# Kernel optimization log

Hardware: AMD Instinct MI355X
Metric: run time of the kernel (lower is better)

## Reference

```python
import jax, jax.numpy as jnp
import numpy as np

N_NODES = 50000
N_EDGES = 400000
B = 2
NUM_STEP = 2
# SAGEConv layer dims (in, out): conv1..conv6
LAYER_DIMS = [(64, 128), (128, 64), (64, 32), (32, 32), (64, 64), (128, 64)]


def setup_inputs() -> dict:
    key = jax.random.key(0)
    ks = jax.random.split(key, 4 + 3 * len(LAYER_DIMS))
    inp = {
        "in_feat": jax.random.normal(ks[0], (B, N_NODES, 64), dtype=jnp.float32),
        "src": jax.random.randint(ks[1], (N_EDGES,), 0, N_NODES, dtype=jnp.int32),
        "dst": jax.random.randint(ks[2], (N_EDGES,), 0, N_NODES, dtype=jnp.int32),
    }
    for i, (fin, fout) in enumerate(LAYER_DIMS, start=1):
        scale = jnp.float32(1.0 / np.sqrt(fin))
        inp[f"w_self{i}"] = jax.random.normal(ks[3 * i], (fin, fout), dtype=jnp.float32) * scale
        inp[f"w_neigh{i}"] = jax.random.normal(ks[3 * i + 1], (fin, fout), dtype=jnp.float32) * scale
        inp[f"b{i}"] = jnp.zeros((fout,), dtype=jnp.float32)
    return inp


def reference(in_feat, src, dst,
              w_self1, w_neigh1, b1, w_self2, w_neigh2, b2,
              w_self3, w_neigh3, b3, w_self4, w_neigh4, b4,
              w_self5, w_neigh5, b5, w_self6, w_neigh6, b6):
    # in_feat: [B, N, F] -> internal [N, B, F] (matches torch transpose(0,1))
    h = jnp.transpose(in_feat, (1, 0, 2))
    # in-degree per dst node for mean aggregation (0-degree nodes -> agg 0)
    deg = jax.ops.segment_sum(jnp.ones(src.shape[0], jnp.float32), dst,
                              num_segments=N_NODES)
    deg = jnp.maximum(deg, 1.0)[:, None, None]  # [N,1,1]

    def sage(x, ws, wn, b):
        # DGL SAGEConv (mean): fc_self(h) + fc_neigh(mean_{u in N(v)} h_u) + b
        agg = jax.ops.segment_sum(x[src], dst, num_segments=N_NODES) / deg
        return x @ ws + agg @ wn + b

    for _ in range(NUM_STEP):
        h1 = jax.nn.relu(sage(h, w_self1, w_neigh1, b1))
        h2 = jax.nn.relu(sage(h1, w_self2, w_neigh2, b2))
        h3 = jax.nn.relu(sage(h2, w_self3, w_neigh3, b3))
        h4 = jnp.concatenate(
            [jax.nn.relu(sage(h3, w_self4, w_neigh4, b4)), h3], axis=2)
        h5 = jnp.concatenate(
            [jax.nn.relu(sage(h4, w_self5, w_neigh5, b5)), h4], axis=2)
        h = sage(h5, w_self6, w_neigh6, b6)
    return jnp.transpose(h, (1, 0, 2))
```

## Files before the change

kernel.cpp:

```cpp
#include <hip/hip_runtime.h>

#define NN 50000
#define NE 400000
#define BB 2
#define ROWS (NN * BB)

#define SCAN_CHUNK 1024
#define SCAN_NB ((NN + SCAN_CHUNK - 1) / SCAN_CHUNK)

__device__ inline void fma4(float4& a, float s, const float4& w) {
    a.x = fmaf(s, w.x, a.x); a.y = fmaf(s, w.y, a.y);
    a.z = fmaf(s, w.z, a.z); a.w = fmaf(s, w.w, a.w);
}
__device__ inline void add4(float4& a, const float4& v) {
    a.x += v.x; a.y += v.y; a.z += v.z; a.w += v.w;
}
__device__ inline unsigned bf2(float a, float b) {
    unsigned ua = __float_as_uint(a); ua = (ua + 0x7FFFu + ((ua >> 16) & 1u)) >> 16;
    unsigned ub = __float_as_uint(b); ub = (ub + 0x7FFFu + ((ub >> 16) & 1u)) >> 16;
    return ua | (ub << 16);
}
__device__ inline void bfadd(float4& lo, float4& hi, uint4 v) {
    lo.x += __uint_as_float(v.x << 16); lo.y += __uint_as_float(v.x & 0xFFFF0000u);
    lo.z += __uint_as_float(v.y << 16); lo.w += __uint_as_float(v.y & 0xFFFF0000u);
    hi.x += __uint_as_float(v.z << 16); hi.y += __uint_as_float(v.z & 0xFFFF0000u);
    hi.z += __uint_as_float(v.w << 16); hi.w += __uint_as_float(v.w & 0xFFFF0000u);
}


__global__ void k_hist(const int* __restrict__ dst, int* __restrict__ deg) {
    int e = blockIdx.x * 256 + threadIdx.x;
    if (e < NE) atomicAdd(&deg[dst[e]], 1);
}

__global__ __launch_bounds__(256) void k_scan1(const int* __restrict__ deg,
                                               int* __restrict__ bsum) {
    int b = blockIdx.x, t = threadIdx.x;
    int base = b * SCAN_CHUNK + t * 4;
    int s = 0;
#pragma unroll
    for (int i = 0; i < 4; i++) {
        int idx = base + i;
        if (idx < NN) s += deg[idx];
    }
    for (int d = 32; d; d >>= 1) s += __shfl_down(s, d);
    __shared__ int ws[4];
    if ((t & 63) == 0) ws[t >> 6] = s;
    __syncthreads();
    if (t == 0) bsum[b] = ws[0] + ws[1] + ws[2] + ws[3];
}

__global__ void k_scan2(const int* __restrict__ bsum, int* __restrict__ boff,
                        int* __restrict__ rowoff_last) {
    int lane = threadIdx.x;
    int v = (lane < SCAN_NB) ? bsum[lane] : 0;
    int incl = v;
    for (int d = 1; d < 64; d <<= 1) {
        int o = __shfl_up(incl, d);
        if (lane >= d) incl += o;
    }
    if (lane < SCAN_NB) boff[lane] = incl - v;
    if (lane == 63) rowoff_last[0] = incl;
}

__global__ __launch_bounds__(256) void k_scan3(const int* __restrict__ deg,
                                               const int* __restrict__ boff,
                                               int* __restrict__ rowoff,
                                               int* __restrict__ cursor,
                                               float* __restrict__ rdeg) {
    int b = blockIdx.x, t = threadIdx.x;
    int lane = t & 63, wv = t >> 6;
    int base = b * SCAN_CHUNK + t * 4;
    int dv[4];
    int ts = 0;
#pragma unroll
    for (int i = 0; i < 4; i++) {
        int idx = base + i;
        dv[i] = (idx < NN) ? deg[idx] : 0;
        ts += dv[i];
    }
    int incl = ts;
    for (int d = 1; d < 64; d <<= 1) {
        int o = __shfl_up(incl, d);
        if (lane >= d) incl += o;
    }
    __shared__ int wsum[4];
    if (lane == 63) wsum[wv] = incl;
    __syncthreads();
    int wexc = 0;
    for (int w = 0; w < wv; w++) wexc += wsum[w];
    int run = boff[b] + wexc + (incl - ts);
#pragma unroll
    for (int i = 0; i < 4; i++) {
        int idx = base + i;
        if (idx < NN) {
            rowoff[idx] = run;
            cursor[idx] = run;
            rdeg[idx] = 1.0f / fmaxf((float)dv[i], 1.0f);
            run += dv[i];
        }
    }
}

__global__ void k_fill(const int* __restrict__ src, const int* __restrict__ dst,
                       int* __restrict__ cursor, int* __restrict__ csr) {
    int e = blockIdx.x * 256 + threadIdx.x;
    if (e >= NE) return;
    int pos = atomicAdd(&cursor[dst[e]], 1);
    csr[pos] = src[e];
}


__global__ void k_gather(const float4* __restrict__ x, const int* __restrict__ csr,
                         const int* __restrict__ rowoff, const float* __restrict__ rdeg,
                         float4* __restrict__ out, int w4s,
                         int xns4, int xbs4, int xo4, int op4, int oo4) {
    int t = blockIdx.x * 256 + threadIdx.x;
    int n = t >> w4s, tid = t & ((1 << w4s) - 1);
    if (n >= NN) return;
    int beg = rowoff[n], end = rowoff[n + 1];
    int a0 = xo4 + tid;
    float4 c00 = {0.f,0.f,0.f,0.f}, c01 = {0.f,0.f,0.f,0.f};
    float4 c10 = {0.f,0.f,0.f,0.f}, c11 = {0.f,0.f,0.f,0.f};
    int j = beg;
    for (; j + 4 <= end; j += 4) {
        int s0 = csr[j], s1 = csr[j+1], s2 = csr[j+2], s3 = csr[j+3];
        int b0 = s0 * xns4 + a0, b1 = s1 * xns4 + a0;
        int b2 = s2 * xns4 + a0, b3 = s3 * xns4 + a0;
        float4 p0 = x[b0], q0 = x[b0 + xbs4];
        float4 p1 = x[b1], q1 = x[b1 + xbs4];
        float4 p2 = x[b2], q2 = x[b2 + xbs4];
        float4 p3 = x[b3], q3 = x[b3 + xbs4];
        add4(c00, p0); add4(c10, q0); add4(c01, p1); add4(c11, q1);
        add4(c00, p2); add4(c10, q2); add4(c01, p3); add4(c11, q3);
    }
    for (; j < end; j++) {
        int s = csr[j];
        int b = s * xns4 + a0;
        add4(c00, x[b]); add4(c10, x[b + xbs4]);
    }
    float rd = rdeg[n];
    float4 o0 = {(c00.x+c01.x)*rd, (c00.y+c01.y)*rd, (c00.z+c01.z)*rd, (c00.w+c01.w)*rd};
    float4 o1 = {(c10.x+c11.x)*rd, (c10.y+c11.y)*rd, (c10.z+c11.z)*rd, (c10.w+c11.w)*rd};
    out[(2*n)     * op4 + oo4 + tid] = o0;
    out[(2*n + 1) * op4 + oo4 + tid] = o1;
}

__global__ void k_gather_bf(const uint4* __restrict__ x, const int* __restrict__ csr,
                            const int* __restrict__ rowoff, const float* __restrict__ rdeg,
                            float4* __restrict__ out, int w8s, int op4, int oo4) {
    int t = blockIdx.x * 256 + threadIdx.x;
    int n = t >> w8s, tid = t & ((1 << w8s) - 1);
    if (n >= NN) return;
    int rp8 = 1 << w8s, nrp = 2 << w8s;
    int beg = rowoff[n], end = rowoff[n + 1];
    float4 a0l = {0.f,0.f,0.f,0.f}, a0h = {0.f,0.f,0.f,0.f};
    float4 a1l = {0.f,0.f,0.f,0.f}, a1h = {0.f,0.f,0.f,0.f};
    int j = beg;
    for (; j + 2 <= end; j += 2) {
        int s0 = csr[j], s1 = csr[j+1];
        int b0 = s0 * nrp + tid, b1 = s1 * nrp + tid;
        uint4 p0 = x[b0], q0 = x[b0 + rp8];
        uint4 p1 = x[b1], q1 = x[b1 + rp8];
        bfadd(a0l, a0h, p0); bfadd(a1l, a1h, q0);
        bfadd(a0l, a0h, p1); bfadd(a1l, a1h, q1);
    }
    if (j < end) {
        int s = csr[j];
        int b = s * nrp + tid;
        bfadd(a0l, a0h, x[b]); bfadd(a1l, a1h, x[b + rp8]);
    }
    float rd = rdeg[n];
    float4 o0l = {a0l.x*rd, a0l.y*rd, a0l.z*rd, a0l.w*rd};
    float4 o0h = {a0h.x*rd, a0h.y*rd, a0h.z*rd, a0h.w*rd};
    float4 o1l = {a1l.x*rd, a1l.y*rd, a1l.z*rd, a1l.w*rd};
    float4 o1h = {a1h.x*rd, a1h.y*rd, a1h.z*rd, a1h.w*rd};
    int r0 = (2*n) * op4 + oo4 + 2*tid;
    int r1 = (2*n + 1) * op4 + oo4 + 2*tid;
    out[r0] = o0l; out[r0 + 1] = o0h;
    out[r1] = o1l; out[r1 + 1] = o1h;
}

template<int FIN, int FOUT, int MODE, bool RELU, bool TRANS, int RPT, int NCQ, int CS, bool OBF>
__global__ __launch_bounds__(256) void k_gemm(
    const float* __restrict__ x, const float* __restrict__ agg,
    const float* __restrict__ w0, const float* __restrict__ w1,
    const float* __restrict__ bias, float* __restrict__ out,
    int xns4, int xbs4, int xo4, int apitch4, int aoff4, int ostride4, int ooff4)
{
    constexpr int NQ = FOUT / 4;
    constexpr int NQB = NQ / CS;
    constexpr int TX = NQB / NCQ;
    constexpr int TY = 256 / TX;
    constexpr int TM = TY * RPT;
    constexpr int W4B = FIN * NQB;
    constexpr int NW = (MODE == 1) ? 2 : 1;

    __shared__ float4 wlds[NW * W4B];

    int t = threadIdx.x;
    int cq0 = blockIdx.y * NQB;
    const float4* w0v = (const float4*)w0;
    for (int i = t; i < W4B; i += 256)
        wlds[i] = w0v[(i / NQB) * NQ + cq0 + (i % NQB)];
    if (MODE == 1) {
        const float4* w1v = (const float4*)w1;
        for (int i = t; i < W4B; i += 256)
            wlds[W4B + i] = w1v[(i / NQB) * NQ + cq0 + (i % NQB)];
    }
    __syncthreads();

    int tx = t % TX, ty = t / TX;
    int rbase = blockIdx.x * TM + ty * RPT;

    int xb[RPT], ab[RPT];
#pragma unroll
    for (int i = 0; i < RPT; i++) {
        int r = rbase + i;
        r = r < ROWS ? r : ROWS - 1;
        xb[i] = (r >> 1) * xns4 + (r & 1) * xbs4 + xo4;
        ab[i] = r * apitch4 + aoff4;
    }

    float4 acc[RPT][NCQ];
#pragma unroll
    for (int i = 0; i < RPT; i++)
#pragma unroll
        for (int j = 0; j < NCQ; j++) acc[i][j] = make_float4(0.f, 0.f, 0.f, 0.f);

    const float4* xv4 = (const float4*)x;
    const float4* av4 = (const float4*)agg;

    for (int k4 = 0; k4 < FIN / 4; k4++) {
        float4 wq[4][NCQ], nq[4][NCQ];
#pragma unroll
        for (int u = 0; u < 4; u++)
#pragma unroll
            for (int j = 0; j < NCQ; j++) {
                wq[u][j] = wlds[(k4 * 4 + u) * NQB + tx + j * TX];
                if (MODE == 1) nq[u][j] = wlds[W4B + (k4 * 4 + u) * NQB + tx + j * TX];
            }
#pragma unroll
        for (int i = 0; i < RPT; i++) {
            float4 xv = xv4[xb[i] + k4];
#pragma unroll
            for (int j = 0; j < NCQ; j++) {
                fma4(acc[i][j], xv.x, wq[0][j]); fma4(acc[i][j], xv.y, wq[1][j]);
                fma4(acc[i][j], xv.z, wq[2][j]); fma4(acc[i][j], xv.w, wq[3][j]);
            }
            if (MODE == 1) {
                float4 av = av4[ab[i] + k4];
#pragma unroll
                for (int j = 0; j < NCQ; j++) {
                    fma4(acc[i][j], av.x, nq[0][j]); fma4(acc[i][j], av.y, nq[1][j]);
                    fma4(acc[i][j], av.z, nq[2][j]); fma4(acc[i][j], av.w, nq[3][j]);
                }
            }
        }
    }

    float4 b4[NCQ];
#pragma unroll
    for (int j = 0; j < NCQ; j++) {
        b4[j] = make_float4(0.f, 0.f, 0.f, 0.f);
        if (MODE != 0) b4[j] = *(const float4*)&bias[(cq0 + tx + j * TX) * 4];
    }

#pragma unroll
    for (int i = 0; i < RPT; i++) {
        int r = rbase + i;
        if (r >= ROWS) continue;
#pragma unroll
        for (int j = 0; j < NCQ; j++) {
            int q = cq0 + tx + j * TX;
            float4 v = acc[i][j];
            if (MODE == 2) {
                float4 ag = av4[ab[i] + q];
                add4(v, ag);
            }
            if (MODE != 0) add4(v, b4[j]);
            if (RELU) {
                v.x = fmaxf(v.x, 0.f); v.y = fmaxf(v.y, 0.f);
                v.z = fmaxf(v.z, 0.f); v.w = fmaxf(v.w, 0.f);
            }
            if (OBF) {
                uint2 w; w.x = bf2(v.x, v.y); w.y = bf2(v.z, v.w);
                ((uint2*)out)[r * ostride4 + ooff4 + q] = w;
            } else {
                int oidx;
                if (TRANS) {
                    int n = r >> 1, b = r & 1;
                    oidx = b * (NN * 16) + n * 16 + q;
                } else {
                    oidx = r * ostride4 + ooff4 + q;
                }
                ((float4*)out)[oidx] = v;
            }
        }
    }
}


template<int FIN, int FOUT, int MODE, bool RELU, bool TRANS,
         int RPT = 8, int NCQ = 1, int CS = 1, bool OBF = false>
static void launch_gemm(const float* x, const float* agg, const float* w0, const float* w1,
                        const float* bias, float* out, int xns4, int xbs4, int xo4,
                        int apitch4, int aoff4, int ostride4, int ooff4,
                        hipStream_t stream) {
    constexpr int TM = (256 / (FOUT / 4 / CS / NCQ)) * RPT;
    int nb = (ROWS + TM - 1) / TM;
    k_gemm<FIN, FOUT, MODE, RELU, TRANS, RPT, NCQ, CS, OBF>
        <<<dim3(nb, CS), 256, 0, stream>>>(
        x, agg, w0, w1, bias, out, xns4, xbs4, xo4, apitch4, aoff4, ostride4, ooff4);
}

static void launch_gather(const float* x, const int* csr, const int* rowoff,
                          const float* rdeg, float* aggb, int width,
                          int xns4, int xbs4, int xo4, int op4, int oo4,
                          hipStream_t stream) {
    int w4s = 0;
    while ((1 << w4s) < width / 4) w4s++;
    int gt = NN << w4s;
    k_gather<<<(gt + 255) / 256, 256, 0, stream>>>(
        (const float4*)x, csr, rowoff, rdeg, (float4*)aggb, w4s,
        xns4, xbs4, xo4, op4, oo4);
}

static void launch_gather_bf(const float* z, const int* csr, const int* rowoff,
                             const float* rdeg, float* aggb, int width,
                             int op4, int oo4, hipStream_t stream) {
    int w8s = 0;
    while ((1 << w8s) < width / 8) w8s++;
    int gt = NN << w8s;
    k_gather_bf<<<(gt + 255) / 256, 256, 0, stream>>>(
        (const uint4*)z, csr, rowoff, rdeg, (float4*)aggb, w8s, op4, oo4);
}

extern "C" void kernel_launch(void* const* d_in, const int* in_sizes, int n_in,
                              void* d_out, int out_size, void* d_ws, size_t ws_size,
                              hipStream_t stream) {
    const float* in_feat = (const float*)d_in[0];
    const int* src = (const int*)d_in[1];
    const int* dst = (const int*)d_in[2];
    const float* Ws[6], *Wn[6], *Bi[6];
    for (int i = 0; i < 6; i++) {
        Ws[i] = (const float*)d_in[3 + 3 * i];
        Wn[i] = (const float*)d_in[4 + 3 * i];
        Bi[i] = (const float*)d_in[5 + 3 * i];
    }

    char* ws = (char*)d_ws;
    size_t off = 0;
    auto alloc = [&](size_t bytes) {
        void* p = ws + off;
        off = (off + bytes + 255) & ~(size_t)255;
        return p;
    };
    float* rdeg   = (float*)alloc((size_t)NN * 4);
    int*   deg    = (int*)  alloc((size_t)NN * 4);
    int*   rowoff = (int*)  alloc((size_t)(NN + 1) * 4);
    int*   cursor = (int*)  alloc((size_t)NN * 4);
    int*   csr    = (int*)  alloc((size_t)NE * 4);
    int*   bsum   = (int*)  alloc((size_t)SCAN_NB * 4);
    int*   boff   = (int*)  alloc((size_t)SCAN_NB * 4);
    float* bufH   = (float*)alloc((size_t)ROWS * 64 * 4);
    float* bufA   = (float*)alloc((size_t)ROWS * 128 * 4);
    float* bufB   = (float*)alloc((size_t)ROWS * 128 * 4);
    float* aggb   = (float*)alloc((size_t)ROWS * 64 * 4);
    float* zbuf   = (float*)d_out;

    hipMemsetAsync(deg, 0, (size_t)NN * 4, stream);
    k_hist<<<(NE + 255) / 256, 256, 0, stream>>>(dst, deg);
    k_scan1<<<SCAN_NB, 256, 0, stream>>>(deg, bsum);
    k_scan2<<<1, 64, 0, stream>>>(bsum, boff, rowoff + NN);
    k_scan3<<<SCAN_NB, 256, 0, stream>>>(deg, boff, rowoff, cursor, rdeg);
    k_fill<<<(NE + 255) / 256, 256, 0, stream>>>(src, dst, cursor, csr);

    const int BSTR = NN * 16;

    for (int s = 0; s < 2; s++) {
        int last = (s == 1);
        const float* hx = s ? bufH : in_feat;
        int hns = s ? 32 : 16, hbs = s ? 16 : BSTR;

        launch_gather(hx, csr, rowoff, rdeg, aggb, 64, hns, hbs, 0, 16, 0, stream);
        launch_gemm<64, 128, 1, true, false, 8, 2, 2>(hx, aggb, Ws[0], Wn[0], Bi[0],
                                                      bufA, hns, hbs, 0, 16, 0, 32, 0, stream);

        launch_gemm<128, 64, 0, false, false, 8, 2, 1, true>(
            bufA, nullptr, Wn[1], nullptr, nullptr, zbuf, 64, 32, 0, 0, 0, 16, 0, stream);
        launch_gather_bf(zbuf, csr, rowoff, rdeg, aggb, 64, 16, 0, stream);
        launch_gemm<128, 64, 2, true, false, 8, 2>(bufA, aggb, Ws[1], nullptr, Bi[1],
                                                   bufH, 64, 32, 0, 16, 0, 16, 0, stream);

        launch_gemm<64, 32, 0, false, false, 8, 1, 1, true>(
            bufH, nullptr, Wn[2], nullptr, nullptr, zbuf, 32, 16, 0, 0, 0, 8, 0, stream);
        launch_gather_bf(zbuf, csr, rowoff, rdeg, aggb, 32, 8, 0, stream);
        launch_gemm<64, 32, 2, true, false, 8, 1>(bufH, aggb, Ws[2], nullptr, Bi[2],
                                                  bufB, 32, 16, 0, 8, 0, 32, 24, stream);

        launch_gather(bufB, csr, rowoff, rdeg, aggb, 32, 64, 32, 24, 16, 8, stream);
        launch_gemm<32, 32, 1, true, false, 8, 1>(bufB, aggb, Ws[3], Wn[3], Bi[3],
                                                  bufB, 64, 32, 24, 16, 8, 32, 16, stream);

        launch_gather(bufB, csr, rowoff, rdeg, aggb, 32, 64, 32, 16, 16, 0, stream);
        launch_gemm<64, 64, 1, true, false, 8, 2>(bufB, aggb, Ws[4], Wn[4], Bi[4],
                                                  bufB, 64, 32, 16, 16, 0, 32, 0, stream);

        launch_gemm<128, 64, 0, false, false, 8, 2, 1, true>(
            bufB, nullptr, Wn[5], nullptr, nullptr, zbuf, 64, 32, 0, 0, 0, 16, 0, stream);
        launch_gather_bf(zbuf, csr, rowoff, rdeg, aggb, 64, 16, 0, stream);
        if (last) {
            launch_gemm<128, 64, 2, false, true, 8, 2>(bufB, aggb, Ws[5], nullptr, Bi[5],
                                                       (float*)d_out, 64, 32, 0, 16, 0, 16, 0, stream);
        } else {
            launch_gemm<128, 64, 2, false, false, 8, 2>(bufB, aggb, Ws[5], nullptr, Bi[5],
                                                        bufH, 64, 32, 0, 16, 0, 16, 0, stream);
        }
    }
}
```

Measured before the change: 1.108 ms.

## Gather all neighbor features from bf16 copies written by GEMM epilogues

Drops the fp32 gather kernel. Every neighbor aggregation now reads bf16 packed features: a pack kernel converts the input once, and the GEMM epilogues gain a DUAL mode that also writes a bf16 copy of their output. The aim is to roughly halve the bytes read in the random-access gathers for layers 1, 4 and 5 and for step 2's input. The column-split (CS) grid dimension in the GEMM is also removed. The cost is bf16 rounding in more aggregations plus extra epilogue stores, and bufA is reused as scratch for the bf16 copies.

```diff
diff --git a/kernel.cpp b/kernel.cpp
--- a/kernel.cpp
+++ b/kernel.cpp
@@ -111,64 +111,44 @@
 }
 
 
-__global__ void k_gather(const float4* __restrict__ x, const int* __restrict__ csr,
-                         const int* __restrict__ rowoff, const float* __restrict__ rdeg,
-                         float4* __restrict__ out, int w4s,
-                         int xns4, int xbs4, int xo4, int op4, int oo4) {
+__global__ void k_pack(const float4* __restrict__ in, uint4* __restrict__ out) {
     int t = blockIdx.x * 256 + threadIdx.x;
-    int n = t >> w4s, tid = t & ((1 << w4s) - 1);
-    if (n >= NN) return;
-    int beg = rowoff[n], end = rowoff[n + 1];
-    int a0 = xo4 + tid;
-    float4 c00 = {0.f,0.f,0.f,0.f}, c01 = {0.f,0.f,0.f,0.f};
-    float4 c10 = {0.f,0.f,0.f,0.f}, c11 = {0.f,0.f,0.f,0.f};
-    int j = beg;
-    for (; j + 4 <= end; j += 4) {
-        int s0 = csr[j], s1 = csr[j+1], s2 = csr[j+2], s3 = csr[j+3];
-        int b0 = s0 * xns4 + a0, b1 = s1 * xns4 + a0;
-        int b2 = s2 * xns4 + a0, b3 = s3 * xns4 + a0;
-        float4 p0 = x[b0], q0 = x[b0 + xbs4];
-        float4 p1 = x[b1], q1 = x[b1 + xbs4];
-        float4 p2 = x[b2], q2 = x[b2 + xbs4];
-        float4 p3 = x[b3], q3 = x[b3 + xbs4];
-        add4(c00, p0); add4(c10, q0); add4(c01, p1); add4(c11, q1);
-        add4(c00, p2); add4(c10, q2); add4(c01, p3); add4(c11, q3);
-    }
-    for (; j < end; j++) {
-        int s = csr[j];
-        int b = s * xns4 + a0;
-        add4(c00, x[b]); add4(c10, x[b + xbs4]);
-    }
-    float rd = rdeg[n];
-    float4 o0 = {(c00.x+c01.x)*rd, (c00.y+c01.y)*rd, (c00.z+c01.z)*rd, (c00.w+c01.w)*rd};
-    float4 o1 = {(c10.x+c11.x)*rd, (c10.y+c11.y)*rd, (c10.z+c11.z)*rd, (c10.w+c11.w)*rd};
-    out[(2*n)     * op4 + oo4 + tid] = o0;
-    out[(2*n + 1) * op4 + oo4 + tid] = o1;
+    if (t >= ROWS * 8) return;
+    int r = t >> 3, k = t & 7;
+    int n = r >> 1, b = r & 1;
+    float4 a = in[(b * NN + n) * 16 + k * 2];
+    float4 c = in[(b * NN + n) * 16 + k * 2 + 1];
+    uint4 o;
+    o.x = bf2(a.x, a.y); o.y = bf2(a.z, a.w);
+    o.z = bf2(c.x, c.y); o.w = bf2(c.z, c.w);
+    out[t] = o;
 }
 
 __global__ void k_gather_bf(const uint4* __restrict__ x, const int* __restrict__ csr,
                             const int* __restrict__ rowoff, const float* __restrict__ rdeg,
-                            float4* __restrict__ out, int w8s, int op4, int oo4) {
+                            float4* __restrict__ out, int w8s, int xp8, int xo8,
+                            int op4, int oo4) {
     int t = blockIdx.x * 256 + threadIdx.x;
     int n = t >> w8s, tid = t & ((1 << w8s) - 1);
     if (n >= NN) return;
-    int rp8 = 1 << w8s, nrp = 2 << w8s;
     int beg = rowoff[n], end = rowoff[n + 1];
+    int a0 = xo8 + tid;
+    int xp2 = 2 * xp8;
     float4 a0l = {0.f,0.f,0.f,0.f}, a0h = {0.f,0.f,0.f,0.f};
     float4 a1l = {0.f,0.f,0.f,0.f}, a1h = {0.f,0.f,0.f,0.f};
     int j = beg;
     for (; j + 2 <= end; j += 2) {
         int s0 = csr[j], s1 = csr[j+1];
-        int b0 = s0 * nrp + tid, b1 = s1 * nrp + tid;
-        uint4 p0 = x[b0], q0 = x[b0 + rp8];
-        uint4 p1 = x[b1], q1 = x[b1 + rp8];
+        int b0 = s0 * xp2 + a0, b1 = s1 * xp2 + a0;
+        uint4 p0 = x[b0], q0 = x[b0 + xp8];
+        uint4 p1 = x[b1], q1 = x[b1 + xp8];
         bfadd(a0l, a0h, p0); bfadd(a1l, a1h, q0);
         bfadd(a0l, a0h, p1); bfadd(a1l, a1h, q1);
     }
     if (j < end) {
         int s = csr[j];
-        int b = s * nrp + tid;
-        bfadd(a0l, a0h, x[b]); bfadd(a1l, a1h, x[b + rp8]);
+        int b = s * xp2 + a0;
+        bfadd(a0l, a0h, x[b]); bfadd(a1l, a1h, x[b + xp8]);
     }
     float rd = rdeg[n];
     float4 o0l = {a0l.x*rd, a0l.y*rd, a0l.z*rd, a0l.w*rd};
@@ -181,32 +161,29 @@
     out[r1] = o1l; out[r1 + 1] = o1h;
 }
 
-template<int FIN, int FOUT, int MODE, bool RELU, bool TRANS, int RPT, int NCQ, int CS, bool OBF>
+template<int FIN, int FOUT, int MODE, bool RELU, bool TRANS, int RPT, int NCQ, bool OBF, bool DUAL>
 __global__ __launch_bounds__(256) void k_gemm(
     const float* __restrict__ x, const float* __restrict__ agg,
     const float* __restrict__ w0, const float* __restrict__ w1,
     const float* __restrict__ bias, float* __restrict__ out,
-    int xns4, int xbs4, int xo4, int apitch4, int aoff4, int ostride4, int ooff4)
+    int xns4, int xbs4, int xo4, int apitch4, int aoff4, int ostride4, int ooff4,
+    uint2* __restrict__ bfo, int bfp2, int bfo2)
 {
     constexpr int NQ = FOUT / 4;
-    constexpr int NQB = NQ / CS;
-    constexpr int TX = NQB / NCQ;
+    constexpr int TX = NQ / NCQ;
     constexpr int TY = 256 / TX;
     constexpr int TM = TY * RPT;
-    constexpr int W4B = FIN * NQB;
+    constexpr int W4 = FIN * NQ;
     constexpr int NW = (MODE == 1) ? 2 : 1;
 
-    __shared__ float4 wlds[NW * W4B];
+    __shared__ float4 wlds[NW * W4];
 
     int t = threadIdx.x;
-    int cq0 = blockIdx.y * NQB;
     const float4* w0v = (const float4*)w0;
-    for (int i = t; i < W4B; i += 256)
-        wlds[i] = w0v[(i / NQB) * NQ + cq0 + (i % NQB)];
+    for (int i = t; i < W4; i += 256) wlds[i] = w0v[i];
     if (MODE == 1) {
         const float4* w1v = (const float4*)w1;
-        for (int i = t; i < W4B; i += 256)
-            wlds[W4B + i] = w1v[(i / NQB) * NQ + cq0 + (i % NQB)];
+        for (int i = t; i < W4; i += 256) wlds[W4 + i] = w1v[i];
     }
     __syncthreads();
 
@@ -237,8 +214,8 @@
         for (int u = 0; u < 4; u++)
 #pragma unroll
             for (int j = 0; j < NCQ; j++) {
-                wq[u][j] = wlds[(k4 * 4 + u) * NQB + tx + j * TX];
-                if (MODE == 1) nq[u][j] = wlds[W4B + (k4 * 4 + u) * NQB + tx + j * TX];
+                wq[u][j] = wlds[(k4 * 4 + u) * NQ + tx + j * TX];
+                if (MODE == 1) nq[u][j] = wlds[W4 + (k4 * 4 + u) * NQ + tx + j * TX];
             }
 #pragma unroll
         for (int i = 0; i < RPT; i++) {
@@ -263,7 +240,7 @@
 #pragma unroll
     for (int j = 0; j < NCQ; j++) {
         b4[j] = make_float4(0.f, 0.f, 0.f, 0.f);
-        if (MODE != 0) b4[j] = *(const float4*)&bias[(cq0 + tx + j * TX) * 4];
+        if (MODE != 0) b4[j] = *(const float4*)&bias[(tx + j * TX) * 4];
     }
 
 #pragma unroll
@@ -272,7 +249,7 @@
         if (r >= ROWS) continue;
 #pragma unroll
         for (int j = 0; j < NCQ; j++) {
-            int q = cq0 + tx + j * TX;
+            int q = tx + j * TX;
             float4 v = acc[i][j];
             if (MODE == 2) {
                 float4 ag = av4[ab[i] + q];
@@ -296,44 +273,37 @@
                 }
                 ((float4*)out)[oidx] = v;
             }
+            if (DUAL) {
+                uint2 w; w.x = bf2(v.x, v.y); w.y = bf2(v.z, v.w);
+                bfo[r * bfp2 + bfo2 + q] = w;
+            }
         }
     }
 }
 
 
 template<int FIN, int FOUT, int MODE, bool RELU, bool TRANS,
-         int RPT = 8, int NCQ = 1, int CS = 1, bool OBF = false>
+         int RPT = 8, int NCQ = 1, bool OBF = false, bool DUAL = false>
 static void launch_gemm(const float* x, const float* agg, const float* w0, const float* w1,
                         const float* bias, float* out, int xns4, int xbs4, int xo4,
                         int apitch4, int aoff4, int ostride4, int ooff4,
-                        hipStream_t stream) {
-    constexpr int TM = (256 / (FOUT / 4 / CS / NCQ)) * RPT;
+                        hipStream_t stream,
+                        uint2* bfo = nullptr, int bfp2 = 0, int bfo2 = 0) {
+    constexpr int TM = (256 / (FOUT / 4 / NCQ)) * RPT;
     int nb = (ROWS + TM - 1) / TM;
-    k_gemm<FIN, FOUT, MODE, RELU, TRANS, RPT, NCQ, CS, OBF>
-        <<<dim3(nb, CS), 256, 0, stream>>>(
-        x, agg, w0, w1, bias, out, xns4, xbs4, xo4, apitch4, aoff4, ostride4, ooff4);
-}
-
-static void launch_gather(const float* x, const int* csr, const int* rowoff,
-                          const float* rdeg, float* aggb, int width,
-                          int xns4, int xbs4, int xo4, int op4, int oo4,
-                          hipStream_t stream) {
-    int w4s = 0;
-    while ((1 << w4s) < width / 4) w4s++;
-    int gt = NN << w4s;
-    k_gather<<<(gt + 255) / 256, 256, 0, stream>>>(
-        (const float4*)x, csr, rowoff, rdeg, (float4*)aggb, w4s,
-        xns4, xbs4, xo4, op4, oo4);
-}
-
-static void launch_gather_bf(const float* z, const int* csr, const int* rowoff,
+    k_gemm<FIN, FOUT, MODE, RELU, TRANS, RPT, NCQ, OBF, DUAL><<<nb, 256, 0, stream>>>(
+        x, agg, w0, w1, bias, out, xns4, xbs4, xo4, apitch4, aoff4, ostride4, ooff4,
+        bfo, bfp2, bfo2);
+}
+
+static void launch_gather_bf(const void* xbf, const int* csr, const int* rowoff,
                              const float* rdeg, float* aggb, int width,
-                             int op4, int oo4, hipStream_t stream) {
+                             int xp8, int xo8, int op4, int oo4, hipStream_t stream) {
     int w8s = 0;
     while ((1 << w8s) < width / 8) w8s++;
     int gt = NN << w8s;
     k_gather_bf<<<(gt + 255) / 256, 256, 0, stream>>>(
-        (const uint4*)z, csr, rowoff, rdeg, (float4*)aggb, w8s, op4, oo4);
+        (const uint4*)xbf, csr, rowoff, rdeg, (float4*)aggb, w8s, xp8, xo8, op4, oo4);
 }
 
 extern "C" void kernel_launch(void* const* d_in, const int* in_sizes, int n_in,
@@ -369,6 +339,9 @@
     float* aggb   = (float*)alloc((size_t)ROWS * 64 * 4);
     float* zbuf   = (float*)d_out;
 
+    uint2* hbf  = (uint2*)bufA;
+    uint2* b3bf = (uint2*)(bufA + (size_t)ROWS * 32);
+
     hipMemsetAsync(deg, 0, (size_t)NN * 4, stream);
     k_hist<<<(NE + 255) / 256, 256, 0, stream>>>(dst, deg);
     k_scan1<<<SCAN_NB, 256, 0, stream>>>(deg, bsum);
@@ -376,6 +349,8 @@
     k_scan3<<<SCAN_NB, 256, 0, stream>>>(deg, boff, rowoff, cursor, rdeg);
     k_fill<<<(NE + 255) / 256, 256, 0, stream>>>(src, dst, cursor, csr);
 
+    k_pack<<<(ROWS * 8 + 255) / 256, 256, 0, stream>>>((const float4*)in_feat, (uint4*)hbf);
+
     const int BSTR = NN * 16;
 
     for (int s = 0; s < 2; s++) {
@@ -383,39 +358,42 @@
         const float* hx = s ? bufH : in_feat;
         int hns = s ? 32 : 16, hbs = s ? 16 : BSTR;
 
-        launch_gather(hx, csr, rowoff, rdeg, aggb, 64, hns, hbs, 0, 16, 0, stream);
-        launch_gemm<64, 128, 1, true, false, 8, 2, 2>(hx, aggb, Ws[0], Wn[0], Bi[0],
-                                                      bufA, hns, hbs, 0, 16, 0, 32, 0, stream);
-
-        launch_gemm<128, 64, 0, false, false, 8, 2, 1, true>(
+        launch_gather_bf(hbf, csr, rowoff, rdeg, aggb, 64, 8, 0, 16, 0, stream);
+        launch_gemm<64, 128, 1, true, false, 8, 2>(hx, aggb, Ws[0], Wn[0], Bi[0],
+                                                   bufA, hns, hbs, 0, 16, 0, 32, 0, stream);
+
+        launch_gemm<128, 64, 0, false, false, 8, 2, true>(
             bufA, nullptr, Wn[1], nullptr, nullptr, zbuf, 64, 32, 0, 0, 0, 16, 0, stream);
-        launch_gather_bf(zbuf, csr, rowoff, rdeg, aggb, 64, 16, 0, stream);
+        launch_gather_bf(zbuf, csr, rowoff, rdeg, aggb, 64, 8, 0, 16, 0, stream);
         launch_gemm<128, 64, 2, true, false, 8, 2>(bufA, aggb, Ws[1], nullptr, Bi[1],
                                                    bufH, 64, 32, 0, 16, 0, 16, 0, stream);
 
-        launch_gemm<64, 32, 0, false, false, 8, 1, 1, true>(
+        launch_gemm<64, 32, 0, false, false, 8, 1, true>(
             bufH, nullptr, Wn[2], nullptr, nullptr, zbuf, 32, 16, 0, 0, 0, 8, 0, stream);
-        launch_gather_bf(zbuf, csr, rowoff, rdeg, aggb, 32, 8, 0, stream);
-        launch_gemm<64, 32, 2, true, false, 8, 1>(bufH, aggb, Ws[2], nullptr, Bi[2],
-                                                  bufB, 32, 16, 0, 8, 0, 32, 24, stream);
-
-        launch_gather(bufB, csr, rowoff, rdeg, aggb, 32, 64, 32, 24, 16, 8, stream);
-        launch_gemm<32, 32, 1, true, false, 8, 1>(bufB, aggb, Ws[3], Wn[3], Bi[3],
-                                                  bufB, 64, 32, 24, 16, 8, 32, 16, stream);
-
-        launch_gather(bufB, csr, rowoff, rdeg, aggb, 32, 64, 32, 16, 16, 0, stream);
+        launch_gather_bf(zbuf, csr, rowoff, rdeg, aggb, 32, 4, 0, 8, 0, stream);
+        launch_gemm<64, 32, 2, true, false, 8, 1, false, true>(
+            bufH, aggb, Ws[2], nullptr, Bi[2], bufB, 32, 16, 0, 8, 0, 32, 24, stream,
+            b3bf, 16, 8);
+
+        launch_gather_bf(b3bf, csr, rowoff, rdeg, aggb, 32, 8, 4, 16, 8, stream);
+        launch_gemm<32, 32, 1, true, false, 8, 1, false, true>(
+            bufB, aggb, Ws[3], Wn[3], Bi[3], bufB, 64, 32, 24, 16, 8, 32, 16, stream,
+            b3bf, 16, 0);
+
+        launch_gather_bf(b3bf, csr, rowoff, rdeg, aggb, 32, 8, 0, 16, 0, stream);
         launch_gemm<64, 64, 1, true, false, 8, 2>(bufB, aggb, Ws[4], Wn[4], Bi[4],
                                                   bufB, 64, 32, 16, 16, 0, 32, 0, stream);
 
-        launch_gemm<128, 64, 0, false, false, 8, 2, 1, true>(
+        launch_gemm<128, 64, 0, false, false, 8, 2, true>(
             bufB, nullptr, Wn[5], nullptr, nullptr, zbuf, 64, 32, 0, 0, 0, 16, 0, stream);
-        launch_gather_bf(zbuf, csr, rowoff, rdeg, aggb, 64, 16, 0, stream);
+        launch_gather_bf(zbuf, csr, rowoff, rdeg, aggb, 64, 8, 0, 16, 0, stream);
         if (last) {
             launch_gemm<128, 64, 2, false, true, 8, 2>(bufB, aggb, Ws[5], nullptr, Bi[5],
                                                        (float*)d_out, 64, 32, 0, 16, 0, 16, 0, stream);
         } else {
-            launch_gemm<128, 64, 2, false, false, 8, 2>(bufB, aggb, Ws[5], nullptr, Bi[5],
-                                                        bufH, 64, 32, 0, 16, 0, 16, 0, stream);
+            launch_gemm<128, 64, 2, false, false, 8, 2, false, true>(
+                bufB, aggb, Ws[5], nullptr, Bi[5], bufH, 64, 32, 0, 16, 0, 16, 0, stream,
+                hbf, 16, 0);
         }
     }
 }
```

Result: faster. 977.1 us (-11.8%).
